# Kernel optimization log

Hardware: AMD Instinct MI355X
Metric: run time of the kernel (lower is better)

The kernel has to match this reference:

```python
import jax, jax.numpy as jnp
import numpy as np

S, B, C = 7, 2, 20
LAMBDA_COORD = 5.0
LAMBDA_NOOBJ = 0.5
EPS = 1e-6


def _to_abs_xyxy(boxes):
    # boxes: [..., S, S, 4] cell-relative (x,y,w,h) -> normalized image (x1,y1,x2,y2)
    col = jnp.arange(S, dtype=boxes.dtype)            # broadcasts over last grid axis
    row = jnp.arange(S, dtype=boxes.dtype)[:, None]   # broadcasts over second-to-last grid axis
    x, y, w, h = boxes[..., 0], boxes[..., 1], boxes[..., 2], boxes[..., 3]
    cx = (col + x) / S
    cy = (row + y) / S
    return jnp.stack([cx - w / 2, cy - h / 2, cx + w / 2, cy + h / 2], axis=-1)


def _iou(a, b):
    # elementwise IoU of corresponding xyxy boxes (broadcasting allowed)
    x1 = jnp.maximum(a[..., 0], b[..., 0])
    y1 = jnp.maximum(a[..., 1], b[..., 1])
    x2 = jnp.minimum(a[..., 2], b[..., 2])
    y2 = jnp.minimum(a[..., 3], b[..., 3])
    inter = jnp.clip(x2 - x1, 0.0) * jnp.clip(y2 - y1, 0.0)
    area_a = (a[..., 2] - a[..., 0]) * (a[..., 3] - a[..., 1])
    area_b = (b[..., 2] - b[..., 0]) * (b[..., 3] - b[..., 1])
    return inter / (area_a + area_b - inter + EPS)


def setup_inputs() -> dict:
    key = jax.random.key(0)
    kp, kb, kf, kc = jax.random.split(key, 4)
    bs = 16384
    predictions = jax.random.uniform(kp, (bs, S, S, B * 5 + C), dtype=jnp.float32)
    gt_box = jax.random.uniform(kb, (bs, S, S, 4), dtype=jnp.float32)
    obj = (jax.random.uniform(kf, (bs, S, S)) < 0.06).astype(jnp.float32)
    cls = jax.nn.one_hot(jax.random.randint(kc, (bs, S, S), 0, C), C, dtype=jnp.float32)
    targets = jnp.concatenate([gt_box, obj[..., None], cls], axis=-1)
    return {"predictions": predictions, "targets": targets}


def reference(predictions, targets):
    bs = predictions.shape[0]
    pb = predictions[..., : B * 5].reshape(bs, S, S, B, 5)
    boxes = pb[..., :4]                 # [bs,S,S,B,4]
    confs = pb[..., 4]                  # [bs,S,S,B]
    logits = predictions[..., B * 5 :]  # [bs,S,S,C]

    gt_boxes = targets[..., :4]
    objf = (targets[..., 4] > 0).astype(predictions.dtype)  # [bs,S,S]
    gt_cls = targets[..., 5:]

    # IoU per candidate box vs the cell's GT box
    gt_abs = _to_abs_xyxy(gt_boxes)                         # [bs,S,S,4]
    pred_abs = _to_abs_xyxy(jnp.moveaxis(boxes, 3, 1))      # [bs,B,S,S,4]
    ious = jnp.moveaxis(_iou(pred_abs, gt_abs[:, None]), 1, 3)  # [bs,S,S,B]

    best = jnp.argmax(ious, axis=-1)                        # [bs,S,S]
    resp_box = jnp.take_along_axis(boxes, best[..., None, None], axis=3)[..., 0, :]  # [bs,S,S,4]
    resp_conf = jnp.take_along_axis(confs, best[..., None], axis=-1)[..., 0]
    resp_iou = jnp.take_along_axis(ious, best[..., None], axis=-1)[..., 0]

    # Localization loss (masked-sum == torch boolean-mask + sum reduction)
    w = objf[..., None]
    xy_loss = jnp.sum(w * (resp_box[..., :2] - gt_boxes[..., :2]) ** 2)
    wh_loss = jnp.sum(w * (jnp.sqrt(resp_box[..., 2:4] + EPS) - jnp.sqrt(gt_boxes[..., 2:4] + EPS)) ** 2)
    loss_coord = xy_loss + wh_loss

    # Objectness confidence: target is (detached) IoU of responsible box
    loss_conf_obj = jnp.sum(objf * (resp_conf - jax.lax.stop_gradient(resp_iou)) ** 2)

    # No-object confidence: every (cell, box) that is not the responsible box of an object cell
    resp_mask = jax.nn.one_hot(best, B, dtype=predictions.dtype) * objf[..., None]  # [bs,S,S,B]
    loss_conf_noobj = jnp.sum((1.0 - resp_mask) * confs ** 2)

    # Classification: cross-entropy with one-hot GT, summed over object cells
    logp = jax.nn.log_softmax(logits, axis=-1)
    loss_class = -jnp.sum(objf * jnp.sum(gt_cls * logp, axis=-1))

    n = jnp.asarray(bs, predictions.dtype)
    loss_total = (LAMBDA_COORD * loss_coord + loss_conf_obj + LAMBDA_NOOBJ * loss_conf_noobj + loss_class) / n
    # [loss_coord, loss_conf_obj, loss_conf_noobj, loss_class, loss_total]
    return jnp.stack([loss_coord / n, loss_conf_obj / n, loss_conf_noobj / n, loss_class / n, loss_total])
```

## Files before the change

kernel.cpp:

```cpp
#include <hip/hip_runtime.h>
#include <math.h>

namespace {
constexpr int S = 7;
constexpr int B = 2;
constexpr int C = 20;
constexpr int PF = B * 5 + C;
constexpr int TF = 5 + C;
constexpr float EPS = 1e-6f;
constexpr float LAMBDA_COORD = 5.0f;
constexpr float LAMBDA_NOOBJ = 0.5f;
constexpr int BLK = 256;
}

__global__ __launch_bounds__(BLK) void k_main(const float* __restrict__ pred,
                                              const float* __restrict__ tgt,
                                              float* __restrict__ part,
                                              int n_cells) {
    const int tid = threadIdx.x;
    const int cell = blockIdx.x * BLK + tid;

    float v0 = 0.f, v1 = 0.f, v2 = 0.f, v3 = 0.f;
    if (cell < n_cells) {
        const float* p = pred + (size_t)cell * PF;
        const float* t = tgt + (size_t)cell * TF;

        const float2 p45 = *(const float2*)(p + 4);
        const float2 p89 = *(const float2*)(p + 8);
        const float c0 = p45.x, c1 = p89.y;
        const float t4 = t[4];

        v2 = c0 * c0 + c1 * c1;

        if (t4 > 0.f) {
            const int j = cell % S;
            const int i = (cell / S) % S;
            const float invS = 1.0f / (float)S;

            const float2 p01 = *(const float2*)(p + 0);
            const float2 p23 = *(const float2*)(p + 2);
            const float2 p67 = *(const float2*)(p + 6);
            const float gx = t[0], gy = t[1], gw = t[2], gh = t[3];

            const float gcx = ((float)j + gx) * invS;
            const float gcy = ((float)i + gy) * invS;
            const float gx1 = gcx - gw * 0.5f, gy1 = gcy - gh * 0.5f;
            const float gx2 = gcx + gw * 0.5f, gy2 = gcy + gh * 0.5f;
            const float garea = (gx2 - gx1) * (gy2 - gy1);

            const float bx[B]  = {p01.x, p45.y};
            const float by[B]  = {p01.y, p67.x};
            const float bw_[B] = {p23.x, p67.y};
            const float bh[B]  = {p23.y, p89.x};
            const float cf[B]  = {c0, c1};
            float iou[B];
            #pragma unroll
            for (int b = 0; b < B; ++b) {
                const float cx = ((float)j + bx[b]) * invS;
                const float cy = ((float)i + by[b]) * invS;
                const float x1 = cx - bw_[b] * 0.5f, y1 = cy - bh[b] * 0.5f;
                const float x2 = cx + bw_[b] * 0.5f, y2 = cy + bh[b] * 0.5f;
                const float ix1 = fmaxf(x1, gx1), iy1 = fmaxf(y1, gy1);
                const float ix2 = fminf(x2, gx2), iy2 = fminf(y2, gy2);
                const float inter = fmaxf(ix2 - ix1, 0.f) * fmaxf(iy2 - iy1, 0.f);
                const float parea = (x2 - x1) * (y2 - y1);
                iou[b] = inter / (parea + garea - inter + EPS);
            }
            const int best = (iou[1] > iou[0]) ? 1 : 0;
            const float rconf = cf[best], riou = iou[best];

            const float dx = bx[best] - gx, dy = by[best] - gy;
            const float swd = sqrtf(bw_[best] + EPS) - sqrtf(gw + EPS);
            const float shd = sqrtf(bh[best] + EPS) - sqrtf(gh + EPS);
            v0 = dx*dx + dy*dy + swd*swd + shd*shd;
            const float dc = rconf - riou;
            v1 = dc * dc;
            v2 -= rconf * rconf;

            float se = 0.f, dot = 0.f, sg = 0.f;
            #pragma unroll
            for (int c = 0; c < C; c += 2) {
                const float2 lc = *(const float2*)(p + 10 + c);
                const float g0 = t[5 + c], g1 = t[6 + c];
                se  += __expf(lc.x) + __expf(lc.y);
                dot += g0 * lc.x + g1 * lc.y;
                sg  += g0 + g1;
            }
            v3 = __logf(se) * sg - dot;
        }
    }

    float v[4] = {v0, v1, v2, v3};
    #pragma unroll
    for (int off = 32; off >= 1; off >>= 1) {
        v[0] += __shfl_down(v[0], off, 64);
        v[1] += __shfl_down(v[1], off, 64);
        v[2] += __shfl_down(v[2], off, 64);
        v[3] += __shfl_down(v[3], off, 64);
    }
    __shared__ float red[16];
    const int lane = tid & 63;
    const int wave = tid >> 6;
    if (lane == 0) {
        red[wave * 4 + 0] = v[0];
        red[wave * 4 + 1] = v[1];
        red[wave * 4 + 2] = v[2];
        red[wave * 4 + 3] = v[3];
    }
    __syncthreads();
    if (tid < 4)
        part[blockIdx.x * 4 + tid] =
            red[tid] + red[4 + tid] + red[8 + tid] + red[12 + tid];
}

__global__ __launch_bounds__(BLK) void k_fin(const float* __restrict__ part,
                                             float* __restrict__ out,
                                             int nblk, float n) {
    const int tid = threadIdx.x;
    float a0 = 0.f, a1 = 0.f, a2 = 0.f, a3 = 0.f;
    for (int r = tid; r < nblk; r += BLK) {
        const float4 q = *(const float4*)(part + r * 4);
        a0 += q.x; a1 += q.y; a2 += q.z; a3 += q.w;
    }
    float v[4] = {a0, a1, a2, a3};
    #pragma unroll
    for (int off = 32; off >= 1; off >>= 1) {
        v[0] += __shfl_down(v[0], off, 64);
        v[1] += __shfl_down(v[1], off, 64);
        v[2] += __shfl_down(v[2], off, 64);
        v[3] += __shfl_down(v[3], off, 64);
    }
    __shared__ float red[16];
    const int lane = tid & 63;
    const int wave = tid >> 6;
    if (lane == 0) {
        red[wave * 4 + 0] = v[0];
        red[wave * 4 + 1] = v[1];
        red[wave * 4 + 2] = v[2];
        red[wave * 4 + 3] = v[3];
    }
    __syncthreads();
    if (tid == 0) {
        const float coord  = red[0] + red[4] + red[8] + red[12];
        const float cobj   = red[1] + red[5] + red[9] + red[13];
        const float cnoobj = red[2] + red[6] + red[10] + red[14];
        const float ccls   = red[3] + red[7] + red[11] + red[15];
        const float inv = 1.0f / n;
        out[0] = coord * inv;
        out[1] = cobj * inv;
        out[2] = cnoobj * inv;
        out[3] = ccls * inv;
        out[4] = (LAMBDA_COORD * coord + cobj + LAMBDA_NOOBJ * cnoobj + ccls) * inv;
    }
}

extern "C" void kernel_launch(void* const* d_in, const int* in_sizes, int n_in,
                              void* d_out, int out_size, void* d_ws, size_t ws_size,
                              hipStream_t stream) {
    const float* pred = (const float*)d_in[0];
    const float* tgt  = (const float*)d_in[1];
    float* out  = (float*)d_out;
    float* part = (float*)d_ws;

    const int n_cells = in_sizes[0] / PF;
    const float bs = (float)(n_cells / (S * S));
    const int nblk = (n_cells + BLK - 1) / BLK;

    k_main<<<nblk, BLK, 0, stream>>>(pred, tgt, part, n_cells);
    k_fin<<<1, BLK, 0, stream>>>(part, out, nblk, bs);
}
```

Baseline: 201.6 us.

## Stage prediction block through LDS with coalesced float4 loads

Each block now copies its 256 cells of prediction data (30 floats per cell) into shared memory with coalesced float4 loads, and each thread then reads its own cell from LDS. This replaces the strided per-thread global loads, which waste cache-line bandwidth. The trade-off is that every prediction byte is fetched, including class logits for non-object cells that the old path skipped, and the 30 KB of LDS per block limits occupancy (launch bounds now request 5 blocks). Target reads stay as strided global loads.

```diff
diff --git a/kernel.cpp b/kernel.cpp
--- a/kernel.cpp
+++ b/kernel.cpp
@@ -11,25 +11,38 @@
 constexpr float LAMBDA_COORD = 5.0f;
 constexpr float LAMBDA_NOOBJ = 0.5f;
 constexpr int BLK = 256;
+constexpr int CH = 256;
+constexpr int PREDF = CH * PF;
 }
 
-__global__ __launch_bounds__(BLK) void k_main(const float* __restrict__ pred,
-                                              const float* __restrict__ tgt,
-                                              float* __restrict__ part,
-                                              int n_cells) {
+__global__ __launch_bounds__(BLK, 5) void k_main(const float* __restrict__ pred,
+                                                 const float* __restrict__ tgt,
+                                                 float* __restrict__ part,
+                                                 int n_cells) {
+    __shared__ float lp[PREDF];
+
     const int tid = threadIdx.x;
-    const int cell = blockIdx.x * BLK + tid;
+    const int base = blockIdx.x * CH;
+    const int cells = min(CH, n_cells - base);
+    const float* pblk = pred + (size_t)base * PF;
+    const float* tblk = tgt + (size_t)base * TF;
+
+    float t4 = 0.f;
+    if (tid < cells) t4 = tblk[tid * TF + 4];
+
+    const int nf = cells * PF;
+    for (int o = tid * 4; o < nf; o += BLK * 4) {
+        const float4 q = *(const float4*)(pblk + o);
+        *(float4*)(&lp[o]) = q;
+    }
+    __syncthreads();
 
     float v0 = 0.f, v1 = 0.f, v2 = 0.f, v3 = 0.f;
-    if (cell < n_cells) {
-        const float* p = pred + (size_t)cell * PF;
-        const float* t = tgt + (size_t)cell * TF;
+    if (tid < cells) {
+        const int cell = base + tid;
+        const float* p = lp + tid * PF;
 
-        const float2 p45 = *(const float2*)(p + 4);
-        const float2 p89 = *(const float2*)(p + 8);
-        const float c0 = p45.x, c1 = p89.y;
-        const float t4 = t[4];
-
+        const float c0 = p[4], c1 = p[9];
         v2 = c0 * c0 + c1 * c1;
 
         if (t4 > 0.f) {
@@ -40,7 +53,10 @@
             const float2 p01 = *(const float2*)(p + 0);
             const float2 p23 = *(const float2*)(p + 2);
             const float2 p67 = *(const float2*)(p + 6);
-            const float gx = t[0], gy = t[1], gw = t[2], gh = t[3];
+            const float gx = tblk[tid * TF + 0];
+            const float gy = tblk[tid * TF + 1];
+            const float gw = tblk[tid * TF + 2];
+            const float gh = tblk[tid * TF + 3];
 
             const float gcx = ((float)j + gx) * invS;
             const float gcy = ((float)i + gy) * invS;
@@ -48,10 +64,10 @@
             const float gx2 = gcx + gw * 0.5f, gy2 = gcy + gh * 0.5f;
             const float garea = (gx2 - gx1) * (gy2 - gy1);
 
-            const float bx[B]  = {p01.x, p45.y};
+            const float bx[B]  = {p01.x, p[5]};
             const float by[B]  = {p01.y, p67.x};
             const float bw_[B] = {p23.x, p67.y};
-            const float bh[B]  = {p23.y, p89.x};
+            const float bh[B]  = {p23.y, p[8]};
             const float cf[B]  = {c0, c1};
             float iou[B];
             #pragma unroll
@@ -81,7 +97,8 @@
             #pragma unroll
             for (int c = 0; c < C; c += 2) {
                 const float2 lc = *(const float2*)(p + 10 + c);
-                const float g0 = t[5 + c], g1 = t[6 + c];
+                const float g0 = tblk[tid * TF + 5 + c];
+                const float g1 = tblk[tid * TF + 6 + c];
                 se  += __expf(lc.x) + __expf(lc.y);
                 dot += g0 * lc.x + g1 * lc.y;
                 sg  += g0 + g1;
@@ -164,7 +181,7 @@
 
     const int n_cells = in_sizes[0] / PF;
     const float bs = (float)(n_cells / (S * S));
-    const int nblk = (n_cells + BLK - 1) / BLK;
+    const int nblk = (n_cells + CH - 1) / CH;
 
     k_main<<<nblk, BLK, 0, stream>>>(pred, tgt, part, n_cells);
     k_fin<<<1, BLK, 0, stream>>>(part, out, nblk, bs);
```

After: 204.4 us. No clear change (+1.4%).

## Stream inputs coalesced with float4, compact object cells, then process them sparsely

Applied to the files above, without the earlier changes.

Replaces the one-thread-per-cell kernel, whose loads are strided by the record size, with a single streaming kernel. Some blocks read the predictions as contiguous float4 and sum the squared confidences, while the others scan the targets for the object flag and use wave ballots plus an atomic counter to build a compacted list of object cells. A second kernel gathers only those listed cells to compute the coord, objectness and class terms, and a final kernel combines the partial sums. This aims for fully coalesced bandwidth-bound reads and avoids divergent per-cell work, at the cost of two extra launches (a counter reset and the gather pass), an atomic list build, and a shared-memory fallback kernel used when the workspace is too small.

```diff
diff --git a/kernel.cpp b/kernel.cpp
--- a/kernel.cpp
+++ b/kernel.cpp
@@ -10,48 +10,278 @@
 constexpr float EPS = 1e-6f;
 constexpr float LAMBDA_COORD = 5.0f;
 constexpr float LAMBDA_NOOBJ = 0.5f;
-constexpr int BLK = 256;
-}
-
-__global__ __launch_bounds__(BLK) void k_main(const float* __restrict__ pred,
-                                              const float* __restrict__ tgt,
-                                              float* __restrict__ part,
-                                              int n_cells) {
+
+constexpr int PBLK = 1120;
+constexpr int TBLK = 980;
+constexpr int OBLK = 256;
+
+constexpr int WS_PART1 = 8;
+constexpr int WS_PART2 = 2048;
+constexpr int WS_LIST  = 4096;
+}
+
+__global__ __launch_bounds__(256) void k_stream(const float4* __restrict__ p4,
+                                                const float4* __restrict__ t4,
+                                                int n_cells,
+                                                float* __restrict__ part1,
+                                                unsigned* __restrict__ list,
+                                                unsigned* __restrict__ counter)
+{
+    const int bid = blockIdx.x;
     const int tid = threadIdx.x;
-    const int cell = blockIdx.x * BLK + tid;
-
+
+    if (bid < PBLK) {
+        const int NT = PBLK * 256;
+        const int np = n_cells * PF;
+        const int np4 = np >> 2;
+        int i = bid * 256 + tid;
+        int r = (4 * i) % 30;
+        const int step = (4 * NT) % 30;
+        float acc = 0.f;
+        for (; i < np4; i += NT) {
+            const float4 q = p4[i];
+            acc += ((r == 4) | (r == 9)) ? q.x * q.x : 0.f;
+            acc += ((r == 3) | (r == 8)) ? q.y * q.y : 0.f;
+            acc += ((r == 2) | (r == 7)) ? q.z * q.z : 0.f;
+            acc += ((r == 1) | (r == 6)) ? q.w * q.w : 0.f;
+            r += step; if (r >= 30) r -= 30;
+        }
+        if (bid == 0 && tid == 0) {
+            const float* pf = (const float*)p4;
+            for (int f = np4 * 4; f < np; ++f) {
+                const int pos = f % 30;
+                if (pos == 4 || pos == 9) acc += pf[f] * pf[f];
+            }
+        }
+        #pragma unroll
+        for (int off = 32; off >= 1; off >>= 1) acc += __shfl_down(acc, off, 64);
+        __shared__ float red[4];
+        if ((tid & 63) == 0) red[tid >> 6] = acc;
+        __syncthreads();
+        if (tid == 0) part1[bid] = red[0] + red[1] + red[2] + red[3];
+    } else {
+        const int NT = TBLK * 256;
+        const int nt = n_cells * TF;
+        const int nt4 = nt >> 2;
+        int i = (bid - PBLK) * 256 + tid;
+        int r = (4 * i) % 25;
+        const int step = (4 * NT) % 25;
+        const int lane = tid & 63;
+        for (; i < nt4; i += NT) {
+            const float4 q = t4[i];
+            bool hit = false;
+            int e = 0;
+            if (r >= 1 && r <= 4) {
+                e = 4 - r;
+                const float val = (e == 0) ? q.x : (e == 1) ? q.y
+                                 : (e == 2) ? q.z : q.w;
+                hit = val > 0.f;
+            }
+            const unsigned long long mask = __ballot(hit);
+            if (mask) {
+                const int leader = __ffsll((long long)mask) - 1;
+                unsigned base = 0;
+                if (lane == leader)
+                    base = atomicAdd(counter, (unsigned)__popcll(mask));
+                base = (unsigned)__shfl((int)base, leader, 64);
+                if (hit) {
+                    const int pos = __popcll(mask & ((1ull << lane) - 1ull));
+                    const unsigned f = (unsigned)(4 * i + e);
+                    list[base + pos] = (f - 4u) / 25u;
+                }
+            }
+            r += step; if (r >= 25) r -= 25;
+        }
+        if (bid == PBLK && tid == 0) {
+            const float* tf = (const float*)t4;
+            for (int f = nt4 * 4; f < nt; ++f) {
+                if (f % 25 == 4 && tf[f] > 0.f) {
+                    const unsigned b = atomicAdd(counter, 1u);
+                    list[b] = (unsigned)(f - 4) / 25u;
+                }
+            }
+        }
+    }
+}
+
+__global__ __launch_bounds__(256) void k_obj(const float* __restrict__ pred,
+                                             const float* __restrict__ tgt,
+                                             const unsigned* __restrict__ list,
+                                             const unsigned* __restrict__ counter,
+                                             float* __restrict__ part2)
+{
+    const unsigned count = *counter;
     float v0 = 0.f, v1 = 0.f, v2 = 0.f, v3 = 0.f;
-    if (cell < n_cells) {
+
+    for (unsigned idx = blockIdx.x * 256 + threadIdx.x; idx < count;
+         idx += OBLK * 256) {
+        const unsigned cell = list[idx];
         const float* p = pred + (size_t)cell * PF;
         const float* t = tgt + (size_t)cell * TF;
 
+        const int j = (int)(cell % S);
+        const int i = (int)((cell / S) % S);
+        const float invS = 1.0f / (float)S;
+
+        const float2 p01 = *(const float2*)(p + 0);
+        const float2 p23 = *(const float2*)(p + 2);
         const float2 p45 = *(const float2*)(p + 4);
+        const float2 p67 = *(const float2*)(p + 6);
         const float2 p89 = *(const float2*)(p + 8);
-        const float c0 = p45.x, c1 = p89.y;
-        const float t4 = t[4];
-
+        const float gx = t[0], gy = t[1], gw = t[2], gh = t[3];
+
+        const float gcx = ((float)j + gx) * invS;
+        const float gcy = ((float)i + gy) * invS;
+        const float gx1 = gcx - gw * 0.5f, gy1 = gcy - gh * 0.5f;
+        const float gx2 = gcx + gw * 0.5f, gy2 = gcy + gh * 0.5f;
+        const float garea = (gx2 - gx1) * (gy2 - gy1);
+
+        const float bx[B]  = {p01.x, p45.y};
+        const float by[B]  = {p01.y, p67.x};
+        const float bw_[B] = {p23.x, p67.y};
+        const float bh[B]  = {p23.y, p89.x};
+        const float cf[B]  = {p45.x, p89.y};
+        float iou[B];
+        #pragma unroll
+        for (int b = 0; b < B; ++b) {
+            const float cx = ((float)j + bx[b]) * invS;
+            const float cy = ((float)i + by[b]) * invS;
+            const float x1 = cx - bw_[b] * 0.5f, y1 = cy - bh[b] * 0.5f;
+            const float x2 = cx + bw_[b] * 0.5f, y2 = cy + bh[b] * 0.5f;
+            const float ix1 = fmaxf(x1, gx1), iy1 = fmaxf(y1, gy1);
+            const float ix2 = fminf(x2, gx2), iy2 = fminf(y2, gy2);
+            const float inter = fmaxf(ix2 - ix1, 0.f) * fmaxf(iy2 - iy1, 0.f);
+            const float parea = (x2 - x1) * (y2 - y1);
+            iou[b] = inter / (parea + garea - inter + EPS);
+        }
+        const int best = (iou[1] > iou[0]) ? 1 : 0;
+        const float rconf = cf[best], riou = iou[best];
+
+        const float dx = bx[best] - gx, dy = by[best] - gy;
+        const float swd = sqrtf(bw_[best] + EPS) - sqrtf(gw + EPS);
+        const float shd = sqrtf(bh[best] + EPS) - sqrtf(gh + EPS);
+        v0 += dx * dx + dy * dy + swd * swd + shd * shd;
+        const float dc = rconf - riou;
+        v1 += dc * dc;
+        v2 -= rconf * rconf;
+
+        float se = 0.f, dot = 0.f, sg = 0.f;
+        #pragma unroll
+        for (int c = 0; c < C; c += 2) {
+            const float2 lc = *(const float2*)(p + 10 + c);
+            const float g0 = t[5 + c], g1 = t[6 + c];
+            se  += __expf(lc.x) + __expf(lc.y);
+            dot += g0 * lc.x + g1 * lc.y;
+            sg  += g0 + g1;
+        }
+        v3 += __logf(se) * sg - dot;
+    }
+
+    float v[4] = {v0, v1, v2, v3};
+    #pragma unroll
+    for (int off = 32; off >= 1; off >>= 1) {
+        v[0] += __shfl_down(v[0], off, 64);
+        v[1] += __shfl_down(v[1], off, 64);
+        v[2] += __shfl_down(v[2], off, 64);
+        v[3] += __shfl_down(v[3], off, 64);
+    }
+    __shared__ float red[16];
+    const int lane = threadIdx.x & 63;
+    const int wave = threadIdx.x >> 6;
+    if (lane == 0) {
+        red[wave * 4 + 0] = v[0];
+        red[wave * 4 + 1] = v[1];
+        red[wave * 4 + 2] = v[2];
+        red[wave * 4 + 3] = v[3];
+    }
+    __syncthreads();
+    if (threadIdx.x < 4)
+        part2[blockIdx.x * 4 + threadIdx.x] =
+            red[threadIdx.x] + red[4 + threadIdx.x] +
+            red[8 + threadIdx.x] + red[12 + threadIdx.x];
+}
+
+__global__ void k_zero(unsigned* counter) { *counter = 0u; }
+
+__global__ __launch_bounds__(256) void k_fin2(const float* __restrict__ part1,
+                                              const float* __restrict__ part2,
+                                              float* __restrict__ out, float n)
+{
+    const int tid = threadIdx.x;
+    float a0 = 0.f, a1 = 0.f, a2 = 0.f, a3 = 0.f;
+    for (int r = tid; r < PBLK; r += 256) a2 += part1[r];
+    for (int r = tid; r < OBLK; r += 256) {
+        const float4 q = *(const float4*)(part2 + r * 4);
+        a0 += q.x; a1 += q.y; a2 += q.z; a3 += q.w;
+    }
+    float v[4] = {a0, a1, a2, a3};
+    #pragma unroll
+    for (int off = 32; off >= 1; off >>= 1) {
+        v[0] += __shfl_down(v[0], off, 64);
+        v[1] += __shfl_down(v[1], off, 64);
+        v[2] += __shfl_down(v[2], off, 64);
+        v[3] += __shfl_down(v[3], off, 64);
+    }
+    __shared__ float red[16];
+    const int lane = tid & 63;
+    const int wave = tid >> 6;
+    if (lane == 0) {
+        red[wave * 4 + 0] = v[0];
+        red[wave * 4 + 1] = v[1];
+        red[wave * 4 + 2] = v[2];
+        red[wave * 4 + 3] = v[3];
+    }
+    __syncthreads();
+    if (tid == 0) {
+        const float coord  = red[0] + red[4] + red[8]  + red[12];
+        const float cobj   = red[1] + red[5] + red[9]  + red[13];
+        const float cnoobj = red[2] + red[6] + red[10] + red[14];
+        const float ccls   = red[3] + red[7] + red[11] + red[15];
+        const float inv = 1.0f / n;
+        out[0] = coord * inv;
+        out[1] = cobj * inv;
+        out[2] = cnoobj * inv;
+        out[3] = ccls * inv;
+        out[4] = (LAMBDA_COORD * coord + cobj + LAMBDA_NOOBJ * cnoobj + ccls) * inv;
+    }
+}
+
+__global__ __launch_bounds__(256) void k_main_fb(const float* __restrict__ pred,
+                                                 const float* __restrict__ tgt,
+                                                 float* __restrict__ part,
+                                                 int n_cells) {
+    __shared__ float lp[256 * PF];
+    __shared__ float lt[256 * TF];
+    const int tid = threadIdx.x;
+    const int block0 = blockIdx.x * 256;
+    const int cells = min(256, n_cells - block0);
+    const size_t pbase = (size_t)block0 * PF;
+    const size_t tbase = (size_t)block0 * TF;
+    for (int o = tid; o < cells * PF; o += 256) lp[o] = pred[pbase + o];
+    for (int o = tid; o < cells * TF; o += 256) lt[o] = tgt[tbase + o];
+    __syncthreads();
+
+    float v0 = 0.f, v1 = 0.f, v2 = 0.f, v3 = 0.f;
+    if (tid < cells) {
+        const int cell = block0 + tid;
+        const float* p = lp + tid * PF;
+        const float* t = lt + tid * TF;
+        const float c0 = p[4], c1 = p[9];
         v2 = c0 * c0 + c1 * c1;
-
-        if (t4 > 0.f) {
+        if (t[4] > 0.f) {
             const int j = cell % S;
             const int i = (cell / S) % S;
             const float invS = 1.0f / (float)S;
-
-            const float2 p01 = *(const float2*)(p + 0);
-            const float2 p23 = *(const float2*)(p + 2);
-            const float2 p67 = *(const float2*)(p + 6);
             const float gx = t[0], gy = t[1], gw = t[2], gh = t[3];
-
             const float gcx = ((float)j + gx) * invS;
             const float gcy = ((float)i + gy) * invS;
             const float gx1 = gcx - gw * 0.5f, gy1 = gcy - gh * 0.5f;
             const float gx2 = gcx + gw * 0.5f, gy2 = gcy + gh * 0.5f;
             const float garea = (gx2 - gx1) * (gy2 - gy1);
-
-            const float bx[B]  = {p01.x, p45.y};
-            const float by[B]  = {p01.y, p67.x};
-            const float bw_[B] = {p23.x, p67.y};
-            const float bh[B]  = {p23.y, p89.x};
+            const float bx[B]  = {p[0], p[5]};
+            const float by[B]  = {p[1], p[6]};
+            const float bw_[B] = {p[2], p[7]};
+            const float bh[B]  = {p[3], p[8]};
             const float cf[B]  = {c0, c1};
             float iou[B];
             #pragma unroll
@@ -68,7 +298,6 @@
             }
             const int best = (iou[1] > iou[0]) ? 1 : 0;
             const float rconf = cf[best], riou = iou[best];
-
             const float dx = bx[best] - gx, dy = by[best] - gy;
             const float swd = sqrtf(bw_[best] + EPS) - sqrtf(gw + EPS);
             const float shd = sqrtf(bh[best] + EPS) - sqrtf(gh + EPS);
@@ -76,7 +305,6 @@
             const float dc = rconf - riou;
             v1 = dc * dc;
             v2 -= rconf * rconf;
-
             float se = 0.f, dot = 0.f, sg = 0.f;
             #pragma unroll
             for (int c = 0; c < C; c += 2) {
@@ -89,7 +317,6 @@
             v3 = __logf(se) * sg - dot;
         }
     }
-
     float v[4] = {v0, v1, v2, v3};
     #pragma unroll
     for (int off = 32; off >= 1; off >>= 1) {
@@ -102,23 +329,21 @@
     const int lane = tid & 63;
     const int wave = tid >> 6;
     if (lane == 0) {
-        red[wave * 4 + 0] = v[0];
-        red[wave * 4 + 1] = v[1];
-        red[wave * 4 + 2] = v[2];
-        red[wave * 4 + 3] = v[3];
+        red[wave*4+0] = v[0]; red[wave*4+1] = v[1];
+        red[wave*4+2] = v[2]; red[wave*4+3] = v[3];
     }
     __syncthreads();
     if (tid < 4)
         part[blockIdx.x * 4 + tid] =
-            red[tid] + red[4 + tid] + red[8 + tid] + red[12 + tid];
-}
-
-__global__ __launch_bounds__(BLK) void k_fin(const float* __restrict__ part,
-                                             float* __restrict__ out,
-                                             int nblk, float n) {
+            red[tid] + red[4+tid] + red[8+tid] + red[12+tid];
+}
+
+__global__ __launch_bounds__(256) void k_fin_fb(const float* __restrict__ part,
+                                                float* __restrict__ out,
+                                                int nblk, float n) {
     const int tid = threadIdx.x;
     float a0 = 0.f, a1 = 0.f, a2 = 0.f, a3 = 0.f;
-    for (int r = tid; r < nblk; r += BLK) {
+    for (int r = tid; r < nblk; r += 256) {
         const float4 q = *(const float4*)(part + r * 4);
         a0 += q.x; a1 += q.y; a2 += q.z; a3 += q.w;
     }
@@ -134,15 +359,13 @@
     const int lane = tid & 63;
     const int wave = tid >> 6;
     if (lane == 0) {
-        red[wave * 4 + 0] = v[0];
-        red[wave * 4 + 1] = v[1];
-        red[wave * 4 + 2] = v[2];
-        red[wave * 4 + 3] = v[3];
+        red[wave*4+0] = v[0]; red[wave*4+1] = v[1];
+        red[wave*4+2] = v[2]; red[wave*4+3] = v[3];
     }
     __syncthreads();
     if (tid == 0) {
-        const float coord  = red[0] + red[4] + red[8] + red[12];
-        const float cobj   = red[1] + red[5] + red[9] + red[13];
+        const float coord  = red[0] + red[4] + red[8]  + red[12];
+        const float cobj   = red[1] + red[5] + red[9]  + red[13];
         const float cnoobj = red[2] + red[6] + red[10] + red[14];
         const float ccls   = red[3] + red[7] + red[11] + red[15];
         const float inv = 1.0f / n;
@@ -159,13 +382,29 @@
                               hipStream_t stream) {
     const float* pred = (const float*)d_in[0];
     const float* tgt  = (const float*)d_in[1];
-    float* out  = (float*)d_out;
-    float* part = (float*)d_ws;
+    float* out = (float*)d_out;
+    float* wsf = (float*)d_ws;
 
     const int n_cells = in_sizes[0] / PF;
     const float bs = (float)(n_cells / (S * S));
-    const int nblk = (n_cells + BLK - 1) / BLK;
-
-    k_main<<<nblk, BLK, 0, stream>>>(pred, tgt, part, n_cells);
-    k_fin<<<1, BLK, 0, stream>>>(part, out, nblk, bs);
-}
+
+    const size_t need = ((size_t)WS_LIST + (size_t)n_cells) * 4;
+    if (ws_size >= need) {
+        unsigned* counter = (unsigned*)d_ws;
+        float* part1 = wsf + WS_PART1;
+        float* part2 = wsf + WS_PART2;
+        unsigned* list = (unsigned*)(wsf + WS_LIST);
+
+        k_zero<<<1, 1, 0, stream>>>(counter);
+        k_stream<<<PBLK + TBLK, 256, 0, stream>>>(
+            (const float4*)pred, (const float4*)tgt, n_cells,
+            part1, list, counter);
+        k_obj<<<OBLK, 256, 0, stream>>>(pred, tgt, list, counter, part2);
+        k_fin2<<<1, 256, 0, stream>>>(part1, part2, out, bs);
+    } else {
+        float* part = wsf;
+        const int nblk = (n_cells + 255) / 256;
+        k_main_fb<<<nblk, 256, 0, stream>>>(pred, tgt, part, n_cells);
+        k_fin_fb<<<1, 256, 0, stream>>>(part, out, nblk, bs);
+    }
+}
```

Result: slower. 572.5 us (+184.1%).
